# Kernel optimization log

Measured on AMD Instinct MI355X. Metric: run time of the kernel, lower is better.

## Reference

```python
import jax, jax.numpy as jnp
import numpy as np
import math

B, S, D, H = 2, 2048, 1024, 16
DH = D // H

def setup_inputs() -> dict:
    key = jax.random.key(0)
    k = jax.random.split(key, 6)
    scale = 1.0 / math.sqrt(D)
    x = jax.random.normal(k[0], (B, S, D), jnp.float32)
    mask = jnp.ones((B, S), jnp.int32)
    # torch.nn.Linear weights: [out_features, in_features]
    W_q = jax.random.normal(k[1], (D, D), jnp.float32) * scale
    b_q = jnp.zeros((D,), jnp.float32)
    W_v = jax.random.normal(k[2], (D, D), jnp.float32) * scale
    W_out = jax.random.normal(k[3], (D, D), jnp.float32) * scale
    b_out = jnp.zeros((D,), jnp.float32)
    return {"x": x, "W_q": W_q, "b_q": b_q, "W_v": W_v, "W_out": W_out, "b_out": b_out, "mask": mask}

def reference(x, W_q, b_q, W_v, W_out, b_out, mask):
    inv_sqrt_dh = 1.0 / math.sqrt(DH)
    # q: [B, H, S, DH]
    q = (x @ W_q.T + b_q).reshape(B, S, H, DH).transpose(0, 2, 1, 3)
    # L2-distance attention logits: -(||q_s||^2 - 2 q_s.q_t + ||q_t||^2)/sqrt(dh)
    sq = jnp.sum(q * q, axis=-1)  # [B, H, S]
    qk = jnp.einsum('bhsd,bhtd->bhst', q, q)  # [B, H, S, S]
    logits = -(sq[..., :, None] - 2.0 * qk + sq[..., None, :]) * inv_sqrt_dh
    logits = jnp.where(mask[:, None, None, :] == 0, jnp.float32(-9e15), logits)
    w = jax.nn.softmax(logits, axis=-1)  # [B, H, S, S]
    # W_q_T[h, j, i] = W_q[i, h*DH + j] -> [H, DH, D]
    W_q_T = W_q.reshape(D, H, DH).transpose(1, 2, 0)
    # v[h, i, j] = W_v[i, h*DH + j] -> [H, D, DH]
    v = W_v.reshape(D, H, DH).transpose(1, 0, 2)
    attn = jnp.einsum('bhst,bhtd->bhsd', w, q)          # [B, H, S, DH]
    attn = jnp.einsum('bhsd,hde->bhse', attn, W_q_T)    # [B, H, S, D]
    attn = jnp.einsum('bhse,hef->bhsf', attn, v) * inv_sqrt_dh  # [B, H, S, DH]
    attn = attn.transpose(0, 2, 1, 3).reshape(B, S, D)
    return x + attn @ W_out.T + b_out
```

## Files before the change

kernel.cpp:

```cpp
#include <hip/hip_runtime.h>

#define S_LEN 2048
#define D_DIM 1024
#define NH    16
#define DHEAD 64

typedef float f32x4 __attribute__((ext_vector_type(4)));
typedef __bf16 bf16x8 __attribute__((ext_vector_type(8)));
typedef unsigned short u16;
typedef unsigned int u32;
typedef unsigned short u16x8 __attribute__((ext_vector_type(8)));
typedef unsigned short u16x4 __attribute__((ext_vector_type(4)));

__device__ __forceinline__ u16 f2bf(float f) {
    union { float f; unsigned u; } c; c.f = f;
    unsigned u = c.u + 0x7fffu + ((c.u >> 16) & 1u);
    return (u16)(u >> 16);
}

#if __has_builtin(__builtin_amdgcn_exp2f)
#define EXP2(x) __builtin_amdgcn_exp2f(x)
#else
#define EXP2(x) exp2f(x)
#endif

#define C_QK  0.36067376022224085f
#define C_SQ  0.18033688011112043f

#define MFMA16(a, b, c) __builtin_amdgcn_mfma_f32_16x16x32_bf16((a), (b), (c), 0, 0, 0)

__device__ __forceinline__ u32 pack_bf(float lo, float hi) {
    union { float f; u32 u; } a, b; a.f = lo; b.f = hi;
    return (b.u & 0xFFFF0000u) | (a.u >> 16);
}

__global__ __launch_bounds__(256) void k_cvt(
    const float* __restrict__ x, const float* __restrict__ wq,
    u16* __restrict__ xb, u16* __restrict__ wqb) {
    const int bid = blockIdx.x;
    const float* s; u16* d; size_t base;
    if (bid < 2048) { s = x;  d = xb;  base = (size_t)bid * 2048 + threadIdx.x * 8; }
    else           { s = wq; d = wqb; base = (size_t)(bid - 2048) * 2048 + threadIdx.x * 8; }
    f32x4 a = *(const f32x4*)(s + base);
    f32x4 b = *(const f32x4*)(s + base + 4);
    u16x8 o;
#pragma unroll
    for (int e = 0; e < 4; ++e) { o[e] = f2bf(a[e]); o[e + 4] = f2bf(b[e]); }
    *(u16x8*)(d + base) = o;
}

__global__ __launch_bounds__(256) void k_precomp_M(
    const float* __restrict__ Wq, const float* __restrict__ Wv, float* __restrict__ Mpart) {
    __shared__ float red[4][8][64];
    const int tid = threadIdx.x;
    const int f = tid & 63, ks = tid >> 6;
    const int jg = blockIdx.x, h = blockIdx.y, z = blockIdx.z;
    const float* vcol = Wv + h * DHEAD + f;
    const float* qcol = Wq + h * DHEAD + jg * 8;
    float acc[8];
#pragma unroll
    for (int jj = 0; jj < 8; ++jj) acc[jj] = 0.f;
    const int e0 = z * 256 + ks * 64;
    for (int e = e0; e < e0 + 64; ++e) {
        float v = vcol[(size_t)e * D_DIM];
        const float* qr = qcol + (size_t)e * D_DIM;
#pragma unroll
        for (int jj = 0; jj < 8; ++jj) acc[jj] += qr[jj] * v;
    }
#pragma unroll
    for (int jj = 0; jj < 8; ++jj) red[ks][jj][f] = acc[jj];
    __syncthreads();
    for (int t = tid; t < 512; t += 256) {
        int jj = t >> 6, ff = t & 63;
        float s = red[0][jj][ff] + red[1][jj][ff] + red[2][jj][ff] + red[3][jj][ff];
        Mpart[(size_t)z * (NH * 64 * 64) + ((size_t)(h * 64 + jg * 8 + jj)) * 64 + ff] = s * 0.125f;
    }
}

__global__ __launch_bounds__(256) void k_precomp_W2(
    const float* __restrict__ Mpart, const float* __restrict__ Wout, u16* __restrict__ W2) {
    __shared__ float Ms[64][65];
    __shared__ float Ws[64][65];
    const int tid = threadIdx.x;
    const int ob = blockIdx.x, h = blockIdx.y;
    {
        int rr = tid >> 2, seg = tid & 3;
        const size_t mo = ((size_t)(h * 64 + rr)) * 64 + seg * 16;
        const float* ws = Wout + (size_t)(ob * 64 + rr) * D_DIM + h * DHEAD + seg * 16;
#pragma unroll
        for (int e = 0; e < 16; ++e) {
            Ms[rr][seg * 16 + e] = Mpart[mo + e] + Mpart[mo + e + 65536]
                                 + Mpart[mo + e + 131072] + Mpart[mo + e + 196608];
            Ws[rr][seg * 16 + e] = ws[e];
        }
    }
    __syncthreads();
    int j = tid & 63, o0 = (tid >> 6) * 16;
    for (int oo = o0; oo < o0 + 16; ++oo) {
        float acc = 0.f;
#pragma unroll
        for (int f = 0; f < 64; ++f) acc += Ms[j][f] * Ws[oo][f];
        W2[(size_t)(ob * 64 + oo) * D_DIM + h * DHEAD + j] = f2bf(acc);
    }
}

__global__ __launch_bounds__(512, 4) void k_qproj(
    const u16* __restrict__ xb, const u16* __restrict__ wqb,
    const float* __restrict__ bq, const int* __restrict__ mask,
    u16* __restrict__ Qbf, u16* __restrict__ QT, float* __restrict__ sq05) {
    __shared__ __align__(16) char smem[38912];
    u16* Al = (u16*)smem;
    u16* Bl = (u16*)(smem + 18432);
    float* sqp = (float*)(smem + 36864);

    const int tid = threadIdx.x, lane = tid & 63, w = tid >> 6;
    const int wm = w & 1, wn = w >> 1;
    const int col16 = lane & 15, quad = lane >> 4;
    const int bm = blockIdx.x, bn = blockIdx.y;

    f32x4 acc[4][2];
    const f32x4 z4 = {0.f, 0.f, 0.f, 0.f};
#pragma unroll
    for (int i = 0; i < 4; ++i)
#pragma unroll
        for (int j = 0; j < 2; ++j) acc[i][j] = z4;

    const int ar = tid >> 2, as = tid & 3;
    const u16* pa = xb + (size_t)(bm * 128 + ar) * D_DIM + as * 16;
    const u16* pb = wqb + (size_t)(bn * 128 + ar) * D_DIM + as * 16;

    u16x8 ra[2], rb[2];
#pragma unroll
    for (int i = 0; i < 2; ++i) ra[i] = *(const u16x8*)(pa + i * 8);
#pragma unroll
    for (int i = 0; i < 2; ++i) rb[i] = *(const u16x8*)(pb + i * 8);

    for (int k0 = 0; k0 < D_DIM; k0 += 64) {
        __syncthreads();
#pragma unroll
        for (int i = 0; i < 2; ++i) *(u16x8*)&Al[ar * 72 + as * 16 + i * 8] = ra[i];
#pragma unroll
        for (int i = 0; i < 2; ++i) *(u16x8*)&Bl[ar * 72 + as * 16 + i * 8] = rb[i];
        __syncthreads();
        if (k0 + 64 < D_DIM) {
#pragma unroll
            for (int i = 0; i < 2; ++i) ra[i] = *(const u16x8*)(pa + k0 + 64 + i * 8);
#pragma unroll
            for (int i = 0; i < 2; ++i) rb[i] = *(const u16x8*)(pb + k0 + 64 + i * 8);
        }
#pragma unroll
        for (int kh = 0; kh < 2; ++kh) {
            bf16x8 af[4];
#pragma unroll
            for (int mt = 0; mt < 4; ++mt)
                af[mt] = *(const bf16x8*)&Al[(wm * 64 + mt * 16 + col16) * 72 + kh * 32 + quad * 8];
#pragma unroll
            for (int nt = 0; nt < 2; ++nt) {
                bf16x8 bfr = *(const bf16x8*)&Bl[(wn * 32 + nt * 16 + col16) * 72 + kh * 32 + quad * 8];
#pragma unroll
                for (int mt = 0; mt < 4; ++mt)
                    acc[mt][nt] = MFMA16(af[mt], bfr, acc[mt][nt]);
            }
        }
    }

    const int hh = wn >> 1;
    f32x4 ssum[4];
#pragma unroll
    for (int mt = 0; mt < 4; ++mt) ssum[mt] = z4;

    u16 qv16[2][4][4];
#pragma unroll
    for (int nt = 0; nt < 2; ++nt) {
        int col = bn * 128 + wn * 32 + nt * 16 + col16;
        float bqv = bq[col];
#pragma unroll
        for (int mt = 0; mt < 4; ++mt) {
            int row0 = bm * 128 + wm * 64 + mt * 16 + quad * 4;
#pragma unroll
            for (int rr = 0; rr < 4; ++rr) {
                float qv = acc[mt][nt][rr] + bqv;
                ssum[mt][rr] += qv * qv;
                u16 bv = f2bf(qv);
                qv16[nt][mt][rr] = bv;
                Qbf[(size_t)(row0 + rr) * D_DIM + col] = bv;
            }
        }
    }
    float vred[4][4];
#pragma unroll
    for (int mt = 0; mt < 4; ++mt)
#pragma unroll
        for (int rr = 0; rr < 4; ++rr) {
            float v = ssum[mt][rr];
            v += __shfl_xor(v, 1); v += __shfl_xor(v, 2);
            v += __shfl_xor(v, 4); v += __shfl_xor(v, 8);
            vred[mt][rr] = v;
        }
    if (col16 == 0) {
#pragma unroll
        for (int mt = 0; mt < 4; ++mt)
#pragma unroll
            for (int rr = 0; rr < 4; ++rr)
                sqp[wn * 128 + wm * 64 + mt * 16 + quad * 4 + rr] = vred[mt][rr];
    }
    __syncthreads();

    u16* Td = (u16*)smem;
#pragma unroll
    for (int nt = 0; nt < 2; ++nt) {
        int dloc = (wn & 1) * 32 + nt * 16 + col16;
#pragma unroll
        for (int mt = 0; mt < 4; ++mt) {
            int sl = wm * 64 + mt * 16 + quad * 4;
#pragma unroll
            for (int rr = 0; rr < 4; ++rr)
                Td[(hh * 64 + dloc) * 130 + sl + rr] = qv16[nt][mt][rr];
        }
    }
    __syncthreads();

    const int bb = (bm * 128) >> 11, s0 = (bm * 128) & 2047;
    if (tid < 256) {
        int r = tid & 127, hh2 = tid >> 7;
        float v = sqp[(2 * hh2) * 128 + r] + sqp[(2 * hh2 + 1) * 128 + r];
        int sidx = s0 + r;
        float o = mask[bb * S_LEN + sidx] ? v * C_SQ : 1e30f;
        sq05[((size_t)(bb * NH + bn * 2 + hh2)) * S_LEN + sidx] = o;
    }
    {
        int dr = tid >> 2, ch = tid & 3;
        int hh3 = dr >> 6, d = dr & 63;
        u16* dst = QT + ((size_t)(bb * NH + bn * 2 + hh3) * DHEAD + d) * S_LEN + s0 + ch * 32;
        const u16* src = Td + (hh3 * 64 + d) * 130 + ch * 32;
#pragma unroll
        for (int i = 0; i < 4; ++i)
            *(u16x8*)(dst + i * 8) = *(const u16x8*)(src + i * 8);
    }
}

__global__ __launch_bounds__(256, 2) void k_flash(
    const u16* __restrict__ Qbf, const u16* __restrict__ QT,
    const float* __restrict__ sq05, u16* __restrict__ attnO) {
    __shared__ __align__(16) char smem[34816];
    u16* Kt  = (u16*)smem;
    u16* KtT = (u16*)(smem + 16384);
    float* sql = (float*)(smem + 32768);

    const int tid = threadIdx.x, lane = tid & 63, w = tid >> 6;
    const int col16 = lane & 15, quad = lane >> 4;
    const int wq = w & 1, wk = w >> 1;
    const int bh = blockIdx.x & 31;
    const int qt = blockIdx.x >> 5;
    const int h = bh & 15;
    const int b = bh >> 4;
    const u16* qbase = Qbf + (size_t)b * S_LEN * D_DIM + h * DHEAD;
    const u16* qtbase = QT + ((size_t)(b * NH + h)) * DHEAD * S_LEN;
    const float* sqb = sq05 + ((size_t)(b * NH + h)) * S_LEN;

    bf16x8 qb[4][2];
#pragma unroll
    for (int nq = 0; nq < 4; ++nq)
#pragma unroll
        for (int k0 = 0; k0 < 2; ++k0)
            qb[nq][k0] = *(const bf16x8*)(qbase +
                (size_t)(qt * 128 + wq * 64 + nq * 16 + col16) * D_DIM + k0 * 32 + quad * 8);

    const int r00 = wk * 64 + (col16 >> 2) * 8 + (col16 & 3);
    const int swzA = (col16 & 3) | (((col16 >> 2) & 1) << 2);
    const int krow00 = r00 * 64 + (quad ^ swzA) * 8;
    const int sq00 = wk * 64 + quad * 8;
    int vrow[4];
#pragma unroll
    for (int dblk = 0; dblk < 4; ++dblk) {
        int rT = dblk * 16 + col16;
        vrow[dblk] = rT * 128 + ((wk * 8 + quad) ^ (rT & 7)) * 8;
    }

    const int kr = tid >> 1, ks = tid & 1;
    const int td = tid >> 2, ts = tid & 3;
    const int kswz = (kr & 3) | (((kr >> 3) & 1) << 2);
    const int tswz = td & 7;
    const u16* ksrc = qbase + (size_t)kr * D_DIM + ks * 32;
    const u16* tsrc = qtbase + (size_t)td * S_LEN + ts * 32;

    u16x8 pk[4], pt[4];
    float sv = 0.f;
#pragma unroll
    for (int i = 0; i < 4; ++i) pk[i] = *(const u16x8*)(ksrc + i * 8);
#pragma unroll
    for (int i = 0; i < 4; ++i) pt[i] = *(const u16x8*)(tsrc + i * 8);
    if (tid < 128) sv = sqb[tid];

    f32x4 Oacc[4][4], lacc[4];
    const f32x4 z4 = {0.f, 0.f, 0.f, 0.f};
#pragma unroll
    for (int n = 0; n < 4; ++n) {
        lacc[n] = z4;
#pragma unroll
        for (int d = 0; d < 4; ++d) Oacc[d][n] = z4;
    }
    bf16x8 ones;
    {
        union { u16x8 u; bf16x8 b; } cv;
#pragma unroll
        for (int e = 0; e < 8; ++e) cv.u[e] = 0x3F80;
        ones = cv.b;
    }

    for (int j = 0; j < S_LEN / 128; ++j) {
        __syncthreads();
#pragma unroll
        for (int i = 0; i < 4; ++i)
            *(u16x8*)(Kt + kr * 64 + ((ks * 4 + i) ^ kswz) * 8) = pk[i];
#pragma unroll
        for (int i = 0; i < 4; ++i)
            *(u16x8*)(KtT + td * 128 + ((ts * 4 + i) ^ tswz) * 8) = pt[i];
        if (tid < 128) sql[tid] = sv;
        __syncthreads();

        int jn = (j + 1) & 15;
        {
            const u16* kn = ksrc + (size_t)jn * 128 * D_DIM;
            const u16* tn = tsrc + (size_t)jn * 128;
#pragma unroll
            for (int i = 0; i < 4; ++i) pk[i] = *(const u16x8*)(kn + i * 8);
#pragma unroll
            for (int i = 0; i < 4; ++i) pt[i] = *(const u16x8*)(tn + i * 8);
            if (tid < 128) sv = sqb[jn * 128 + tid];
        }

        for (int kt = 0; kt < 2; ++kt) {
            f32x4 sacc[2][4];
#pragma unroll
            for (int kbh = 0; kbh < 2; ++kbh)
#pragma unroll
                for (int nq = 0; nq < 4; ++nq) sacc[kbh][nq] = z4;
#pragma unroll
            for (int kbh = 0; kbh < 2; ++kbh) {
                int kro = krow00 + kt * 2048 + kbh * 256;
                bf16x8 a0 = *(const bf16x8*)(Kt + kro);
                bf16x8 a1 = *(const bf16x8*)(Kt + (kro ^ 32));
#pragma unroll
                for (int nq = 0; nq < 4; ++nq) {
                    sacc[kbh][nq] = MFMA16(a0, qb[nq][0], sacc[kbh][nq]);
                    sacc[kbh][nq] = MFMA16(a1, qb[nq][1], sacc[kbh][nq]);
                }
            }

            bf16x8 va[4];
#pragma unroll
            for (int dblk = 0; dblk < 4; ++dblk)
                va[dblk] = *(const bf16x8*)(KtT + (vrow[dblk] ^ (kt * 32)));

            u32 pf[4][4];
#pragma unroll
            for (int kbh = 0; kbh < 2; ++kbh) {
                f32x4 sqv = *(const f32x4*)(sql + sq00 + kt * 32 + kbh * 4);
#pragma unroll
                for (int nq = 0; nq < 4; ++nq) {
                    float p0 = EXP2(fmaf(sacc[kbh][nq][0], C_QK, -sqv[0]));
                    float p1 = EXP2(fmaf(sacc[kbh][nq][1], C_QK, -sqv[1]));
                    float p2 = EXP2(fmaf(sacc[kbh][nq][2], C_QK, -sqv[2]));
                    float p3 = EXP2(fmaf(sacc[kbh][nq][3], C_QK, -sqv[3]));
                    pf[nq][kbh * 2]     = pack_bf(p0, p1);
                    pf[nq][kbh * 2 + 1] = pack_bf(p2, p3);
                }
            }

#pragma unroll
            for (int nq = 0; nq < 4; ++nq) {
                union { u32 u[4]; bf16x8 b; } pb;
#pragma unroll
                for (int i = 0; i < 4; ++i) pb.u[i] = pf[nq][i];
                lacc[nq] = MFMA16(ones, pb.b, lacc[nq]);
#pragma unroll
                for (int dblk = 0; dblk < 4; ++dblk)
                    Oacc[dblk][nq] = MFMA16(va[dblk], pb.b, Oacc[dblk][nq]);
            }
        }
    }

    __syncthreads();
    float* Obuf = (float*)smem;
    float* lred = (float*)(smem + 32768);
    if (wk == 1) {
#pragma unroll
        for (int dblk = 0; dblk < 4; ++dblk)
#pragma unroll
            for (int nq = 0; nq < 4; ++nq)
                *(f32x4*)(Obuf + ((wq * 16 + dblk * 4 + nq) * 64 + lane) * 4) = Oacc[dblk][nq];
#pragma unroll
        for (int nq = 0; nq < 4; ++nq)
            lred[(wq * 4 + nq) * 64 + lane] = lacc[nq][0];
    }
    __syncthreads();
    if (wk == 0) {
        float rinv[4];
#pragma unroll
        for (int nq = 0; nq < 4; ++nq)
            rinv[nq] = 1.f / (lacc[nq][0] + lred[(wq * 4 + nq) * 64 + lane]);
        u16* obase = attnO + (size_t)b * S_LEN * D_DIM + h * DHEAD;
#pragma unroll
        for (int dblk = 0; dblk < 4; ++dblk)
#pragma unroll
            for (int nq = 0; nq < 4; ++nq) {
                f32x4 o = Oacc[dblk][nq] + *(const f32x4*)(Obuf + ((wq * 16 + dblk * 4 + nq) * 64 + lane) * 4);
                int q = qt * 128 + wq * 64 + nq * 16 + col16;
                u16x4 pkk;
#pragma unroll
                for (int rr = 0; rr < 4; ++rr) pkk[rr] = f2bf(o[rr] * rinv[nq]);
                *(u16x4*)(obase + (size_t)q * D_DIM + dblk * 16 + quad * 4) = pkk;
            }
    }
}

__global__ __launch_bounds__(512, 4) void k_oproj(
    const u16* __restrict__ attnO, const u16* __restrict__ W2,
    const float* __restrict__ x, const float* __restrict__ bout, float* __restrict__ out) {
    __shared__ __align__(16) char smem[36864];
    u16* Al = (u16*)smem;
    u16* Bl = (u16*)(smem + 18432);
    const int tid = threadIdx.x, lane = tid & 63, w = tid >> 6;
    const int wm = w & 1, wn = w >> 1;
    const int col16 = lane & 15, quad = lane >> 4;
    const int bm = blockIdx.x, bn = blockIdx.y;

    f32x4 acc[4][2];
    const f32x4 z4 = {0.f, 0.f, 0.f, 0.f};
#pragma unroll
    for (int i = 0; i < 4; ++i)
#pragma unroll
        for (int j = 0; j < 2; ++j) acc[i][j] = z4;

    const int ar = tid >> 2, as = tid & 3;
    const u16* pa = attnO + (size_t)(bm * 128 + ar) * D_DIM + as * 16;
    const u16* pb = W2 + (size_t)(bn * 128 + ar) * D_DIM + as * 16;

    u16x8 ra[2], rb[2];
#pragma unroll
    for (int i = 0; i < 2; ++i) ra[i] = *(const u16x8*)(pa + i * 8);
#pragma unroll
    for (int i = 0; i < 2; ++i) rb[i] = *(const u16x8*)(pb + i * 8);

    for (int k0 = 0; k0 < D_DIM; k0 += 64) {
        __syncthreads();
#pragma unroll
        for (int i = 0; i < 2; ++i) *(u16x8*)&Al[ar * 72 + as * 16 + i * 8] = ra[i];
#pragma unroll
        for (int i = 0; i < 2; ++i) *(u16x8*)&Bl[ar * 72 + as * 16 + i * 8] = rb[i];
        __syncthreads();
        if (k0 + 64 < D_DIM) {
#pragma unroll
            for (int i = 0; i < 2; ++i) ra[i] = *(const u16x8*)(pa + k0 + 64 + i * 8);
#pragma unroll
            for (int i = 0; i < 2; ++i) rb[i] = *(const u16x8*)(pb + k0 + 64 + i * 8);
        }
#pragma unroll
        for (int kh = 0; kh < 2; ++kh) {
            bf16x8 af[4];
#pragma unroll
            for (int mt = 0; mt < 4; ++mt)
                af[mt] = *(const bf16x8*)&Al[(wm * 64 + mt * 16 + col16) * 72 + kh * 32 + quad * 8];
#pragma unroll
            for (int nt = 0; nt < 2; ++nt) {
                bf16x8 bfr = *(const bf16x8*)&Bl[(wn * 32 + nt * 16 + col16) * 72 + kh * 32 + quad * 8];
#pragma unroll
                for (int mt = 0; mt < 4; ++mt)
                    acc[mt][nt] = MFMA16(af[mt], bfr, acc[mt][nt]);
            }
        }
    }
#pragma unroll
    for (int nt = 0; nt < 2; ++nt) {
        int col = bn * 128 + wn * 32 + nt * 16 + col16;
        float bv = bout[col];
#pragma unroll
        for (int mt = 0; mt < 4; ++mt) {
            int row0 = bm * 128 + wm * 64 + mt * 16 + quad * 4;
#pragma unroll
            for (int rr = 0; rr < 4; ++rr) {
                size_t idx = (size_t)(row0 + rr) * D_DIM + col;
                out[idx] = acc[mt][nt][rr] + x[idx] + bv;
            }
        }
    }
}

extern "C" void kernel_launch(void* const* d_in, const int* in_sizes, int n_in,
                              void* d_out, int out_size, void* d_ws, size_t ws_size,
                              hipStream_t stream) {
    const float* x    = (const float*)d_in[0];
    const float* Wq   = (const float*)d_in[1];
    const float* bq   = (const float*)d_in[2];
    const float* Wv   = (const float*)d_in[3];
    const float* Wout = (const float*)d_in[4];
    const float* bout = (const float*)d_in[5];
    const int*   mask = (const int*)d_in[6];
    float* out = (float*)d_out;

    char* ws = (char*)d_ws;
    u16*   Qbf   = (u16*)(ws);
    u16*   QT    = (u16*)(ws + (8u << 20));
    u16*   xb    = (u16*)(ws + (16u << 20));
    u16*   wqb   = (u16*)(ws + (24u << 20));
    u16*   W2    = (u16*)(ws + (26u << 20));
    float* Mpart = (float*)(ws + (28u << 20));
    float* sq05  = (float*)(ws + (29u << 20));
    u16*   attnO = xb;

    k_cvt<<<dim3(2560), dim3(256), 0, stream>>>(x, Wq, xb, wqb);
    k_precomp_M<<<dim3(8, 16, 4), dim3(256), 0, stream>>>(Wq, Wv, Mpart);
    k_precomp_W2<<<dim3(16, 16), dim3(256), 0, stream>>>(Mpart, Wout, W2);
    k_qproj<<<dim3(32, 8), dim3(512), 0, stream>>>(xb, wqb, bq, mask, Qbf, QT, sq05);
    k_flash<<<dim3(512), dim3(256), 0, stream>>>(Qbf, QT, sq05, attnO);
    k_oproj<<<dim3(32, 8), dim3(512), 0, stream>>>(attnO, W2, x, bout, out);
}
```

Measured before the change: 203.0 us.

## Fuse fp32-to-bf16 conversion into Q projection and retile M precompute

Removes the separate conversion kernel: the Q-projection GEMM now loads fp32 x and W_q directly and converts to bf16 in registers before staging into shared memory. This drops one launch and the extra write and read of bf16 copies, but doubles the global bytes loaded per tile inside the GEMM loop. The W_q^T·W_v precompute is also rewritten to stage 128-row slabs of both matrices in shared memory and compute 4x4 register tiles, producing 8 partial sums instead of 4, with the W2 kernel summing all 8.

```diff
diff --git a/kernel.cpp b/kernel.cpp
--- a/kernel.cpp
+++ b/kernel.cpp
@@ -34,46 +34,41 @@
     return (b.u & 0xFFFF0000u) | (a.u >> 16);
 }
 
-__global__ __launch_bounds__(256) void k_cvt(
-    const float* __restrict__ x, const float* __restrict__ wq,
-    u16* __restrict__ xb, u16* __restrict__ wqb) {
-    const int bid = blockIdx.x;
-    const float* s; u16* d; size_t base;
-    if (bid < 2048) { s = x;  d = xb;  base = (size_t)bid * 2048 + threadIdx.x * 8; }
-    else           { s = wq; d = wqb; base = (size_t)(bid - 2048) * 2048 + threadIdx.x * 8; }
-    f32x4 a = *(const f32x4*)(s + base);
-    f32x4 b = *(const f32x4*)(s + base + 4);
-    u16x8 o;
-#pragma unroll
-    for (int e = 0; e < 4; ++e) { o[e] = f2bf(a[e]); o[e + 4] = f2bf(b[e]); }
-    *(u16x8*)(d + base) = o;
-}
-
 __global__ __launch_bounds__(256) void k_precomp_M(
     const float* __restrict__ Wq, const float* __restrict__ Wv, float* __restrict__ Mpart) {
-    __shared__ float red[4][8][64];
+    __shared__ float Qp[128][64];
+    __shared__ float Vp[128][64];
     const int tid = threadIdx.x;
-    const int f = tid & 63, ks = tid >> 6;
-    const int jg = blockIdx.x, h = blockIdx.y, z = blockIdx.z;
-    const float* vcol = Wv + h * DHEAD + f;
-    const float* qcol = Wq + h * DHEAD + jg * 8;
-    float acc[8];
-#pragma unroll
-    for (int jj = 0; jj < 8; ++jj) acc[jj] = 0.f;
-    const int e0 = z * 256 + ks * 64;
-    for (int e = e0; e < e0 + 64; ++e) {
-        float v = vcol[(size_t)e * D_DIM];
-        const float* qr = qcol + (size_t)e * D_DIM;
-#pragma unroll
-        for (int jj = 0; jj < 8; ++jj) acc[jj] += qr[jj] * v;
-    }
-#pragma unroll
-    for (int jj = 0; jj < 8; ++jj) red[ks][jj][f] = acc[jj];
+    const int z = blockIdx.x, h = blockIdx.y;
+    {
+        int r = tid >> 1, hf = tid & 1;
+        const float* q = Wq + (size_t)(z * 128 + r) * D_DIM + h * DHEAD + hf * 32;
+        const float* v = Wv + (size_t)(z * 128 + r) * D_DIM + h * DHEAD + hf * 32;
+#pragma unroll
+        for (int i = 0; i < 8; ++i) {
+            *(f32x4*)&Qp[r][hf * 32 + i * 4] = *(const f32x4*)(q + i * 4);
+            *(f32x4*)&Vp[r][hf * 32 + i * 4] = *(const f32x4*)(v + i * 4);
+        }
+    }
     __syncthreads();
-    for (int t = tid; t < 512; t += 256) {
-        int jj = t >> 6, ff = t & 63;
-        float s = red[0][jj][ff] + red[1][jj][ff] + red[2][jj][ff] + red[3][jj][ff];
-        Mpart[(size_t)z * (NH * 64 * 64) + ((size_t)(h * 64 + jg * 8 + jj)) * 64 + ff] = s * 0.125f;
+    const int j0 = (tid >> 4) * 4;
+    const int f0 = (tid & 15) * 4;
+    f32x4 acc[4];
+    const f32x4 z4 = {0.f, 0.f, 0.f, 0.f};
+#pragma unroll
+    for (int i = 0; i < 4; ++i) acc[i] = z4;
+    for (int e = 0; e < 128; ++e) {
+        f32x4 qv = *(const f32x4*)&Qp[e][j0];
+        f32x4 vv = *(const f32x4*)&Vp[e][f0];
+#pragma unroll
+        for (int jj = 0; jj < 4; ++jj)
+            acc[jj] += qv[jj] * vv;
+    }
+    float* dst = Mpart + (size_t)z * (NH * 64 * 64) + ((size_t)(h * 64 + j0)) * 64 + f0;
+#pragma unroll
+    for (int jj = 0; jj < 4; ++jj) {
+        f32x4 o = acc[jj] * 0.125f;
+        *(f32x4*)(dst + jj * 64) = o;
     }
 }
 
@@ -89,8 +84,10 @@
         const float* ws = Wout + (size_t)(ob * 64 + rr) * D_DIM + h * DHEAD + seg * 16;
 #pragma unroll
         for (int e = 0; e < 16; ++e) {
-            Ms[rr][seg * 16 + e] = Mpart[mo + e] + Mpart[mo + e + 65536]
-                                 + Mpart[mo + e + 131072] + Mpart[mo + e + 196608];
+            float s = 0.f;
+#pragma unroll
+            for (int k = 0; k < 8; ++k) s += Mpart[mo + e + (size_t)k * 65536];
+            Ms[rr][seg * 16 + e] = s;
             Ws[rr][seg * 16 + e] = ws[e];
         }
     }
@@ -105,7 +102,7 @@
 }
 
 __global__ __launch_bounds__(512, 4) void k_qproj(
-    const u16* __restrict__ xb, const u16* __restrict__ wqb,
+    const float* __restrict__ x, const float* __restrict__ Wq,
     const float* __restrict__ bq, const int* __restrict__ mask,
     u16* __restrict__ Qbf, u16* __restrict__ QT, float* __restrict__ sq05) {
     __shared__ __align__(16) char smem[38912];
@@ -126,27 +123,37 @@
         for (int j = 0; j < 2; ++j) acc[i][j] = z4;
 
     const int ar = tid >> 2, as = tid & 3;
-    const u16* pa = xb + (size_t)(bm * 128 + ar) * D_DIM + as * 16;
-    const u16* pb = wqb + (size_t)(bn * 128 + ar) * D_DIM + as * 16;
-
-    u16x8 ra[2], rb[2];
-#pragma unroll
-    for (int i = 0; i < 2; ++i) ra[i] = *(const u16x8*)(pa + i * 8);
-#pragma unroll
-    for (int i = 0; i < 2; ++i) rb[i] = *(const u16x8*)(pb + i * 8);
+    const float* pa = x + (size_t)(bm * 128 + ar) * D_DIM + as * 16;
+    const float* pb = Wq + (size_t)(bn * 128 + ar) * D_DIM + as * 16;
+
+    f32x4 fa[4], fb[4];
+#pragma unroll
+    for (int i = 0; i < 4; ++i) {
+        fa[i] = *(const f32x4*)(pa + i * 4);
+        fb[i] = *(const f32x4*)(pb + i * 4);
+    }
 
     for (int k0 = 0; k0 < D_DIM; k0 += 64) {
+        u16x8 wa[2], wb[2];
+#pragma unroll
+        for (int i = 0; i < 2; ++i)
+#pragma unroll
+            for (int e = 0; e < 4; ++e) {
+                wa[i][e] = f2bf(fa[2 * i][e]); wa[i][e + 4] = f2bf(fa[2 * i + 1][e]);
+                wb[i][e] = f2bf(fb[2 * i][e]); wb[i][e + 4] = f2bf(fb[2 * i + 1][e]);
+            }
         __syncthreads();
 #pragma unroll
-        for (int i = 0; i < 2; ++i) *(u16x8*)&Al[ar * 72 + as * 16 + i * 8] = ra[i];
-#pragma unroll
-        for (int i = 0; i < 2; ++i) *(u16x8*)&Bl[ar * 72 + as * 16 + i * 8] = rb[i];
+        for (int i = 0; i < 2; ++i) *(u16x8*)&Al[ar * 72 + as * 16 + i * 8] = wa[i];
+#pragma unroll
+        for (int i = 0; i < 2; ++i) *(u16x8*)&Bl[ar * 72 + as * 16 + i * 8] = wb[i];
         __syncthreads();
         if (k0 + 64 < D_DIM) {
 #pragma unroll
-            for (int i = 0; i < 2; ++i) ra[i] = *(const u16x8*)(pa + k0 + 64 + i * 8);
-#pragma unroll
-            for (int i = 0; i < 2; ++i) rb[i] = *(const u16x8*)(pb + k0 + 64 + i * 8);
+            for (int i = 0; i < 4; ++i) {
+                fa[i] = *(const f32x4*)(pa + k0 + 64 + i * 4);
+                fb[i] = *(const f32x4*)(pb + k0 + 64 + i * 4);
+            }
         }
 #pragma unroll
         for (int kh = 0; kh < 2; ++kh) {
@@ -502,17 +509,14 @@
     char* ws = (char*)d_ws;
     u16*   Qbf   = (u16*)(ws);
     u16*   QT    = (u16*)(ws + (8u << 20));
-    u16*   xb    = (u16*)(ws + (16u << 20));
-    u16*   wqb   = (u16*)(ws + (24u << 20));
-    u16*   W2    = (u16*)(ws + (26u << 20));
-    float* Mpart = (float*)(ws + (28u << 20));
-    float* sq05  = (float*)(ws + (29u << 20));
-    u16*   attnO = xb;
-
-    k_cvt<<<dim3(2560), dim3(256), 0, stream>>>(x, Wq, xb, wqb);
-    k_precomp_M<<<dim3(8, 16, 4), dim3(256), 0, stream>>>(Wq, Wv, Mpart);
+    u16*   attnO = (u16*)(ws + (16u << 20));
+    u16*   W2    = (u16*)(ws + (24u << 20));
+    float* Mpart = (float*)(ws + (26u << 20));
+    float* sq05  = (float*)(ws + (28u << 20));
+
+    k_precomp_M<<<dim3(8, 16), dim3(256), 0, stream>>>(Wq, Wv, Mpart);
     k_precomp_W2<<<dim3(16, 16), dim3(256), 0, stream>>>(Mpart, Wout, W2);
-    k_qproj<<<dim3(32, 8), dim3(512), 0, stream>>>(xb, wqb, bq, mask, Qbf, QT, sq05);
+    k_qproj<<<dim3(32, 8), dim3(512), 0, stream>>>(x, Wq, bq, mask, Qbf, QT, sq05);
     k_flash<<<dim3(512), dim3(256), 0, stream>>>(Qbf, QT, sq05, attnO);
     k_oproj<<<dim3(32, 8), dim3(512), 0, stream>>>(attnO, W2, x, bout, out);
 }
```

Result: no change. 204.3 us (+0.6%).
